# Optimization experiments

Hardware: AMD Instinct MI355X
Metric: run time of the kernel (lower is better)

Reference implementation:

```python
import jax, jax.numpy as jnp
import numpy as np

SINKHORN_ALPHA = 0.05
OT_MAX_ITER = 100
STOP_THR = 0.005
EPS = 1e-16
N_TOPICS, VOCAB, DIM = 1024, 50000, 256


def setup_inputs() -> dict:
    key = jax.random.key(0)
    k1, k2 = jax.random.split(key)
    x = jax.random.uniform(k1, (N_TOPICS, DIM), dtype=jnp.float32)
    y = jax.random.uniform(k2, (VOCAB, DIM), dtype=jnp.float32)
    return {"x": x, "y": y}


def _pairwise_sq_euclidean(x, y):
    return (jnp.sum(x * x, axis=1, keepdims=True)
            + jnp.sum(y * y, axis=1)
            - 2.0 * (x @ y.T))


def reference(x, y):
    M = _pairwise_sq_euclidean(x, y)          # [n, m]
    n, m = M.shape
    dt = M.dtype
    a = jnp.full((n, 1), 1.0 / n, dtype=dt)    # uniform source marginal
    b = jnp.full((m, 1), 1.0 / m, dtype=dt)    # uniform target marginal
    K = jnp.exp(-M * SINKHORN_ALPHA)           # Gibbs kernel [n, m]
    u0 = jnp.full((n, 1), 1.0 / n, dtype=dt)
    v0 = jnp.zeros((m, 1), dtype=dt)

    def cond_fn(carry):
        u, v, err, cpt = carry
        return (err > STOP_THR) & (cpt < OT_MAX_ITER)

    def body_fn(carry):
        u, v, err, cpt = carry
        v = b / (K.T @ u + EPS)                # [m, 1]
        u = a / (K @ v + EPS)                  # [n, 1]
        cpt = cpt + 1

        def compute_err(_):
            bb = v * (K.T @ u)                 # current column marginal
            return jnp.max(jnp.sum(jnp.abs(bb - b), axis=0))

        # original: convergence check only when cpt % 50 == 1
        err = jax.lax.cond((cpt % 50) == 1, compute_err, lambda _: err, operand=None)
        return (u, v, err, cpt)

    init = (u0, v0, jnp.asarray(1.0, dt), jnp.asarray(0, jnp.int32))
    u, v, err, cpt = jax.lax.while_loop(cond_fn, body_fn, init)

    transp = u * (K * v.T)                     # transport plan [n, m]
    loss_etp = jnp.sum(transp * M)
    return (loss_etp, transp)
```

## Files before the change

### kernel.cpp

```cpp
#include <hip/hip_runtime.h>
#include <hip/hip_cooperative_groups.h>
#include <cstdint>

namespace cg = cooperative_groups;

#define N_T 1024
#define M_V 50000
#define DIMS 256
#define NPAD 50048
#define GPANELS 391
#define CBLK 196
#define NPART (CBLK * 64)
#define NCHUNK 782
#define COOP_BLOCKS 1024
#define J8TOT 6250
#define F8BLK 25
#define LPART (F8BLK * 64)

constexpr float ALPHA     = 0.05f;
constexpr float INV_ALPHA = 20.0f;
constexpr float A_VAL     = 1.0f / 1024.0f;
constexpr float B_VAL     = 1.0f / 50000.0f;
constexpr float THR       = 0.005f;
constexpr float EPSV      = 1e-16f;

typedef short    bf16x8 __attribute__((ext_vector_type(8)));
typedef float    f32x4  __attribute__((ext_vector_type(4)));
typedef _Float16 half8v __attribute__((ext_vector_type(8)));

__device__ __forceinline__ float blockReduce256(float val) {
  #pragma unroll
  for (int off = 32; off; off >>= 1) val += __shfl_down(val, off, 64);
  __shared__ float redw[4];
  int lane = threadIdx.x & 63;
  int wid  = threadIdx.x >> 6;
  if (lane == 0) redw[wid] = val;
  __syncthreads();
  float r = 0.0f;
  if (threadIdx.x == 0) r = redw[0] + redw[1] + redw[2] + redw[3];
  __syncthreads();
  return r;
}

__device__ __forceinline__ unsigned short f2bf(float f) {
  union { float f; unsigned u; } c{f};
  unsigned r = c.u + 0x7FFF + ((c.u >> 16) & 1);
  return (unsigned short)(r >> 16);
}
__device__ __forceinline__ float bf2f(unsigned short b) {
  union { unsigned u; float f; } c{(unsigned)b << 16};
  return c.f;
}

__device__ __forceinline__ void gload16(const void* g, void* l) {
  __builtin_amdgcn_global_load_lds((const __attribute__((address_space(1))) unsigned int*)g,
                                   (__attribute__((address_space(3))) unsigned int*)l, 16, 0, 0);
}

__global__ __launch_bounds__(256) void sumsq_kernel(const float* __restrict__ in,
                                                    float* __restrict__ o, int rows) {
  int r = blockIdx.x;
  if (r >= rows) return;
  float v = in[(size_t)r * DIMS + threadIdx.x];
  float s = blockReduce256(v * v);
  if (threadIdx.x == 0) o[r] = s;
}

__global__ __launch_bounds__(256) void pack_x_kernel(const float* __restrict__ x,
                                                     unsigned short* __restrict__ Ap,
                                                     float* __restrict__ xx) {
  int r = blockIdx.x * 2 + (threadIdx.x >> 7);
  int k = (threadIdx.x & 127) * 2;
  float2 vx = *(const float2*)&x[(size_t)r * DIMS + k];
  ushort2 h2, l2;
  h2.x = f2bf(vx.x); h2.y = f2bf(vx.y);
  l2.x = f2bf(vx.x - bf2f(h2.x)); l2.y = f2bf(vx.y - bf2f(h2.y));
  *(ushort2*)&Ap[(size_t)r * 512 + k]       = h2;
  *(ushort2*)&Ap[(size_t)r * 512 + 256 + k] = l2;
  float ssq = vx.x * vx.x + vx.y * vx.y;
  #pragma unroll
  for (int off = 32; off; off >>= 1) ssq += __shfl_down(ssq, off, 64);
  __shared__ float rr[4];
  int lane = threadIdx.x & 63, wid = threadIdx.x >> 6;
  if (lane == 0) rr[wid] = ssq;
  __syncthreads();
  if ((threadIdx.x & 127) == 0) xx[r] = rr[wid] + rr[wid + 1];
}

__global__ __launch_bounds__(256) void pack_y_kernel(const float* __restrict__ y,
                                                     unsigned short* __restrict__ Bp,
                                                     float* __restrict__ yy) {
  int r = blockIdx.x * 2 + (threadIdx.x >> 7);
  int k = (threadIdx.x & 127) * 2;
  ushort2 h2 = {0, 0};
  float ssq = 0.0f;
  if (r < M_V) {
    float2 vy = *(const float2*)&y[(size_t)r * DIMS + k];
    h2.x = f2bf(vy.x); h2.y = f2bf(vy.y);
    ssq = vy.x * vy.x + vy.y * vy.y;
  }
  *(ushort2*)&Bp[(size_t)r * 256 + k] = h2;
  #pragma unroll
  for (int off = 32; off; off >>= 1) ssq += __shfl_down(ssq, off, 64);
  __shared__ float rr[4];
  int lane = threadIdx.x & 63, wid = threadIdx.x >> 6;
  if (lane == 0) rr[wid] = ssq;
  __syncthreads();
  if ((threadIdx.x & 127) == 0 && r < M_V) yy[r] = rr[wid] + rr[wid + 1];
}

__global__ __launch_bounds__(256) void mfma_gemm_kernel(const unsigned short* __restrict__ Ap,
                                                        const unsigned short* __restrict__ Bp,
                                                        const float* __restrict__ xx,
                                                        const float* __restrict__ yy,
                                                        _Float16* __restrict__ Kh,
                                                        float* __restrict__ colsumPart) {
  const int t  = blockIdx.x & 63;
  const int gb = blockIdx.x >> 6;
  const int panel = gb * 8 + (t & 7);
  const int rt    = t >> 3;
  if (panel >= GPANELS) return;
  const int i0 = rt * 128;
  const int j0 = panel * 128;

  __shared__ unsigned short Ah[2][128][32];
  __shared__ unsigned short Al[2][128][32];
  __shared__ unsigned short Bs[2][128][32];
  const int tid  = threadIdx.x;
  const int lane = tid & 63;
  const int wid  = tid >> 6;
  const int wr = wid >> 1, wc = wid & 1;

  f32x4 acc[4][4];
  #pragma unroll
  for (int m = 0; m < 4; ++m)
    #pragma unroll
    for (int n = 0; n < 4; ++n) acc[m][n] = (f32x4){0.f, 0.f, 0.f, 0.f};

  const int srow  = lane >> 2;
  const int sslot = lane & 3;

  auto STAGE = [&](int b, int k0) {
    #pragma unroll
    for (int q = 0; q < 2; ++q) {
      int rbase = (wid * 2 + q) * 16;
      int row = rbase + srow;
      int cg_ = sslot ^ ((row >> 1) & 3);
      gload16(Ap + (size_t)(i0 + row) * 512 + k0 + cg_ * 8,       &Ah[b][rbase][0]);
      gload16(Ap + (size_t)(i0 + row) * 512 + 256 + k0 + cg_ * 8, &Al[b][rbase][0]);
      gload16(Bp + (size_t)(j0 + row) * 256 + k0 + cg_ * 8,       &Bs[b][rbase][0]);
    }
  };

  STAGE(0, 0);
  int cur = 0;
  #pragma unroll
  for (int step = 0; step < 8; ++step) {
    if (step < 7) {
      STAGE(cur ^ 1, (step + 1) * 32);
      asm volatile("s_waitcnt vmcnt(6)" ::: "memory");
    } else {
      asm volatile("s_waitcnt vmcnt(0)" ::: "memory");
    }
    __builtin_amdgcn_s_barrier();
    __builtin_amdgcn_sched_barrier(0);
    bf16x8 ah[4], al[4], bb[4];
    #pragma unroll
    for (int m = 0; m < 4; ++m) {
      int row = wr * 64 + m * 16 + (lane & 15);
      int sl  = (lane >> 4) ^ ((row >> 1) & 3);
      ah[m] = *(const bf16x8*)&Ah[cur][row][sl * 8];
      al[m] = *(const bf16x8*)&Al[cur][row][sl * 8];
    }
    #pragma unroll
    for (int n = 0; n < 4; ++n) {
      int col = wc * 64 + n * 16 + (lane & 15);
      int sl  = (lane >> 4) ^ ((col >> 1) & 3);
      bb[n] = *(const bf16x8*)&Bs[cur][col][sl * 8];
    }
    #pragma unroll
    for (int m = 0; m < 4; ++m)
      #pragma unroll
      for (int n = 0; n < 4; ++n) {
        acc[m][n] = __builtin_amdgcn_mfma_f32_16x16x32_bf16(ah[m], bb[n], acc[m][n], 0, 0, 0);
        acc[m][n] = __builtin_amdgcn_mfma_f32_16x16x32_bf16(al[m], bb[n], acc[m][n], 0, 0, 0);
      }
    asm volatile("s_waitcnt lgkmcnt(0)" ::: "memory");
    __builtin_amdgcn_sched_barrier(0);
    __builtin_amdgcn_s_barrier();
    cur ^= 1;
  }

  float csum[4] = {0.f, 0.f, 0.f, 0.f};
  #pragma unroll
  for (int m = 0; m < 4; ++m) {
    int rowb = i0 + wr * 64 + m * 16 + (lane >> 4) * 4;
    #pragma unroll
    for (int n = 0; n < 4; ++n) {
      int col = j0 + wc * 64 + n * 16 + (lane & 15);
      float yyc = (col < M_V) ? yy[col] : 0.0f;
      #pragma unroll
      for (int r = 0; r < 4; ++r) {
        float mval = xx[rowb + r] + yyc - 2.0f * acc[m][n][r];
        _Float16 kh = (_Float16)__expf(-ALPHA * mval);
        if (col < M_V) Kh[(size_t)(rowb + r) * M_V + col] = kh;
        csum[n] += (float)kh;
      }
    }
  }
  #pragma unroll
  for (int n = 0; n < 4; ++n) {
    float c = csum[n];
    c += __shfl_xor(c, 16, 64);
    c += __shfl_xor(c, 32, 64);
    if (lane < 16) {
      int col = j0 + wc * 64 + n * 16 + lane;
      colsumPart[(size_t)(rt * 2 + wr) * NPAD + col] = c;
    }
  }
}

#define BM 64
#define BN 64
#define BK 32
__global__ __launch_bounds__(256) void gemm_k_kernel(const float* __restrict__ x,
                                                     const float* __restrict__ y,
                                                     const float* __restrict__ xx,
                                                     const float* __restrict__ yy,
                                                     float* Kmat) {
  __shared__ float As[BK][BM];
  __shared__ float Bs[BK][BN + 1];
  int tid = threadIdx.x;
  int i0 = blockIdx.y * BM;
  int j0 = blockIdx.x * BN;
  int tx = tid & 15, ty = tid >> 4;
  float acc[4][4] = {};
  for (int k0 = 0; k0 < DIMS; k0 += BK) {
    #pragma unroll
    for (int l = tid; l < 512; l += 256) {
      int r = l >> 3, kq = l & 7;
      float4 a4 = *(const float4*)&x[(size_t)(i0 + r) * DIMS + k0 + kq * 4];
      As[kq * 4 + 0][r] = a4.x; As[kq * 4 + 1][r] = a4.y;
      As[kq * 4 + 2][r] = a4.z; As[kq * 4 + 3][r] = a4.w;
    }
    #pragma unroll
    for (int l = tid; l < 512; l += 256) {
      int r = l >> 3, kq = l & 7;
      int j = j0 + r;
      float4 b4 = make_float4(0.f, 0.f, 0.f, 0.f);
      if (j < M_V) b4 = *(const float4*)&y[(size_t)j * DIMS + k0 + kq * 4];
      Bs[kq * 4 + 0][r] = b4.x; Bs[kq * 4 + 1][r] = b4.y;
      Bs[kq * 4 + 2][r] = b4.z; Bs[kq * 4 + 3][r] = b4.w;
    }
    __syncthreads();
    #pragma unroll
    for (int k = 0; k < BK; ++k) {
      float a[4], b[4];
      #pragma unroll
      for (int r = 0; r < 4; ++r) a[r] = As[k][ty * 4 + r];
      #pragma unroll
      for (int c = 0; c < 4; ++c) b[c] = Bs[k][tx * 4 + c];
      #pragma unroll
      for (int r = 0; r < 4; ++r)
        #pragma unroll
        for (int c = 0; c < 4; ++c) acc[r][c] += a[r] * b[c];
    }
    __syncthreads();
  }
  #pragma unroll
  for (int r = 0; r < 4; ++r) {
    int i = i0 + ty * 4 + r;
    float xxi = xx[i];
    #pragma unroll
    for (int c = 0; c < 4; ++c) {
      int j = j0 + tx * 4 + c;
      if (j < M_V) {
        float m = xxi + yy[j] - 2.0f * acc[r][c];
        Kmat[(size_t)i * M_V + j] = __expf(-ALPHA * m);
      }
    }
  }
}

__global__ __launch_bounds__(256) void v1_kernel(const float* __restrict__ cp,
                                                 float* __restrict__ v,
                                                 float* __restrict__ errAcc) {
  int j = blockIdx.x * 256 + threadIdx.x;
  if (j == 0) errAcc[0] = 0.0f;
  if (j < M_V) {
    float s = 0.0f;
    #pragma unroll
    for (int q = 0; q < 16; ++q) s += cp[(size_t)q * NPAD + j];
    v[j] = B_VAL / (s * A_VAL + EPSV);
  }
}

__global__ __launch_bounds__(256) void rowpass_kernel(const _Float16* __restrict__ Kh,
                                                      const float* __restrict__ v,
                                                      float* __restrict__ rowPart) {
  const int i = blockIdx.y;
  const int c = blockIdx.x;
  const half8v* K8 = (const half8v*)(Kh + (size_t)i * M_V);
  const float4* v4 = (const float4*)v;
  float p = 0.0f;
  int q = c * 3125 + threadIdx.x;
  #pragma unroll
  for (int it = 0; it < 12; ++it, q += 256) {
    half8v k8 = K8[q];
    float4 va = v4[q * 2], vb = v4[q * 2 + 1];
    p += (float)k8[0] * va.x + (float)k8[1] * va.y + (float)k8[2] * va.z + (float)k8[3] * va.w
       + (float)k8[4] * vb.x + (float)k8[5] * vb.y + (float)k8[6] * vb.z + (float)k8[7] * vb.w;
  }
  if (threadIdx.x < 53) {
    int q2 = c * 3125 + 3072 + threadIdx.x;
    half8v k8 = K8[q2];
    float4 va = v4[q2 * 2], vb = v4[q2 * 2 + 1];
    p += (float)k8[0] * va.x + (float)k8[1] * va.y + (float)k8[2] * va.z + (float)k8[3] * va.w
       + (float)k8[4] * vb.x + (float)k8[5] * vb.y + (float)k8[6] * vb.z + (float)k8[7] * vb.w;
  }
  p = blockReduce256(p);
  if (threadIdx.x == 0) rowPart[c * N_T + i] = p;
}

__global__ void u_kernel(const float* __restrict__ rowPart, float* __restrict__ u) {
  int i = blockIdx.x * 256 + threadIdx.x;
  u[i] = A_VAL / (rowPart[i] + rowPart[N_T + i] + EPSV);
}

__global__ __launch_bounds__(256) void specfinal_kernel(const _Float16* __restrict__ Kh,
                                                        const float* __restrict__ u_,
                                                        const float* __restrict__ v_,
                                                        float* __restrict__ out,
                                                        float* __restrict__ sPart,
                                                        float* __restrict__ lossPart) {
  const int j8 = blockIdx.x * 256 + threadIdx.x;
  const int by = blockIdx.y;
  float contrib = 0.0f;
  if (j8 < J8TOT) {
    const size_t jb = (size_t)j8 * 8;
    float4 va = ((const float4*)v_)[j8 * 2];
    float4 vb = ((const float4*)v_)[j8 * 2 + 1];
    float sp0 = 0.f, sp1 = 0.f, sp2 = 0.f, sp3 = 0.f;
    float sp4 = 0.f, sp5 = 0.f, sp6 = 0.f, sp7 = 0.f;
    #pragma unroll
    for (int r = 0; r < 16; ++r) {
      int i = by * 16 + r;
      half8v k8 = *(const half8v*)(Kh + (size_t)i * M_V + jb);
      float ui = u_[i];
      float k0 = (float)k8[0], k1 = (float)k8[1], k2 = (float)k8[2], k3 = (float)k8[3];
      float k4 = (float)k8[4], k5 = (float)k8[5], k6 = (float)k8[6], k7 = (float)k8[7];
      float t0 = ui * k0 * va.x, t1 = ui * k1 * va.y, t2 = ui * k2 * va.z, t3 = ui * k3 * va.w;
      float t4 = ui * k4 * vb.x, t5 = ui * k5 * vb.y, t6 = ui * k6 * vb.z, t7 = ui * k7 * vb.w;
      size_t o = 1 + (size_t)i * M_V + jb;
      out[o]     = t0; out[o + 1] = t1; out[o + 2] = t2; out[o + 3] = t3;
      out[o + 4] = t4; out[o + 5] = t5; out[o + 6] = t6; out[o + 7] = t7;
      contrib += t0 * (-__logf(k0)) + t1 * (-__logf(k1)) + t2 * (-__logf(k2)) + t3 * (-__logf(k3))
               + t4 * (-__logf(k4)) + t5 * (-__logf(k5)) + t6 * (-__logf(k6)) + t7 * (-__logf(k7));
      sp0 += k0 * ui; sp1 += k1 * ui; sp2 += k2 * ui; sp3 += k3 * ui;
      sp4 += k4 * ui; sp5 += k5 * ui; sp6 += k6 * ui; sp7 += k7 * ui;
    }
    float* sb = sPart + (size_t)by * M_V + jb;
    *(float4*)sb       = make_float4(sp0, sp1, sp2, sp3);
    *(float4*)(sb + 4) = make_float4(sp4, sp5, sp6, sp7);
  }
  contrib = blockReduce256(contrib) * INV_ALPHA;
  if (threadIdx.x == 0) lossPart[by * F8BLK + blockIdx.x] = contrib;
}

__global__ __launch_bounds__(256) void errfinish_kernel(const float* __restrict__ sPart,
                                                        const float* __restrict__ v_,
                                                        float* errAcc) {
  int j = blockIdx.x * 256 + threadIdx.x;
  float e = 0.0f;
  if (j < M_V) {
    float s = 0.0f;
    #pragma unroll
    for (int q = 0; q < 64; ++q) s += sPart[(size_t)q * M_V + j];
    e = fabsf(v_[j] * s - B_VAL);
  }
  e = blockReduce256(e);
  if (threadIdx.x == 0) atomicAdd(errAcc, e);
}

__global__ void setflag_kernel(const float* errAcc, int* notconv) {
  *notconv = (errAcc[0] > THR) ? 1 : 0;
}
__global__ void set1_kernel(int* p) { *p = 1; }

__global__ __launch_bounds__(256) void finishloss_kernel(const float* __restrict__ lossPart,
                                                         float* out, int np_) {
  float s = 0.0f;
  for (int i = threadIdx.x; i < np_; i += 256) s += lossPart[i];
  s = blockReduce256(s);
  if (threadIdx.x == 0) out[0] = s;
}

template <typename KT>
__global__ __launch_bounds__(256, 4) void sinkhorn_coop(const KT* Km,
                                                        float* __restrict__ u,
                                                        float* __restrict__ v,
                                                        float* __restrict__ s,
                                                        float* __restrict__ errAcc,
                                                        const int* __restrict__ notconv) {
  if (*notconv == 0) return;
  cg::grid_group grid = cg::this_grid();
  __shared__ float su[N_T];
  __shared__ float red[8][64];
  const int tid = threadIdx.x;
  const int bid = blockIdx.x;
  {
    int g0 = bid * 256 + tid;
    if (g0 < N_T) u[g0] = A_VAL;
    if (g0 < 2) errAcc[g0] = 0.0f;
  }
  grid.sync();
  for (int t = 1; t <= 100; ++t) {
    const bool check = (t == 2) || (t == 52);
    for (int i = tid; i < N_T; i += 256) su[i] = u[i];
    __syncthreads();
    const int g = tid >> 5, jl = tid & 31;
    float eacc = 0.0f;
    for (int c = bid; c < NCHUNK; c += COOP_BLOCKS) {
      const int j0 = c * 64;
      const int jj = j0 + jl * 2;
      float p0 = 0.f, p1 = 0.f;
      if (jj < M_V) {
        const KT* base = Km + (size_t)(g * 128) * M_V + jj;
        #pragma unroll 4
        for (int i = 0; i < 128; ++i) {
          float k0 = (float)base[(size_t)i * M_V];
          float k1 = (float)base[(size_t)i * M_V + 1];
          float uu = su[g * 128 + i];
          p0 += k0 * uu; p1 += k1 * uu;
        }
      }
      red[g][jl * 2]     = p0;
      red[g][jl * 2 + 1] = p1;
      __syncthreads();
      if (tid < 64) {
        int j = j0 + tid;
        if (j < M_V) {
          float st = 0.f;
          #pragma unroll
          for (int q = 0; q < 8; ++q) st += red[q][tid];
          if (check) {
            s[j] = st;
            eacc += fabsf(v[j] * st - B_VAL);
          } else {
            v[j] = B_VAL / (st + EPSV);
          }
        }
      }
      __syncthreads();
    }
    if (check) {
      float e = blockReduce256(eacc);
      if (tid == 0) atomicAdd(&errAcc[t == 2 ? 0 : 1], e);
    }
    grid.sync();
    if (check) {
      float e = errAcc[t == 2 ? 0 : 1];
      if (e <= THR) break;
      if (tid < 64) {
        for (int c = bid; c < NCHUNK; c += COOP_BLOCKS) {
          int j = c * 64 + tid;
          if (j < M_V) v[j] = B_VAL / (s[j] + EPSV);
        }
      }
      grid.sync();
    }
    {
      int i = bid;
      float p = 0.f;
      if (i < N_T) {
        const KT* row = Km + (size_t)i * M_V;
        for (int j = tid; j < M_V; j += 256) p += (float)row[j] * v[j];
      }
      p = blockReduce256(p);
      if (tid == 0 && i < N_T) u[i] = A_VAL / (p + EPSV);
    }
    grid.sync();
  }
}

template <typename KT>
__global__ __launch_bounds__(256) void final_kernel(const KT* Kmat,
                                                    const float* __restrict__ u,
                                                    const float* __restrict__ v,
                                                    float* out,
                                                    float* __restrict__ partials,
                                                    const int* __restrict__ gate) {
  if (*gate == 0) return;
  int j = blockIdx.x * 256 + threadIdx.x;
  float contrib = 0.0f;
  if (j < M_V) {
    float vj = v[j];
    #pragma unroll 4
    for (int r = 0; r < 16; ++r) {
      int i = blockIdx.y * 16 + r;
      size_t idx = (size_t)i * M_V + j;
      float k = (float)Kmat[idx];
      float tr = u[i] * k * vj;
      float m = -__logf(k) * INV_ALPHA;
      out[1 + idx] = tr;
      contrib += tr * m;
    }
  }
  contrib = blockReduce256(contrib);
  if (threadIdx.x == 0) partials[blockIdx.y * gridDim.x + blockIdx.x] = contrib;
}

__global__ __launch_bounds__(256) void finish_kernel(const float* __restrict__ partials,
                                                     float* out, int np_,
                                                     const int* __restrict__ gate) {
  if (*gate == 0) return;
  float s = 0.0f;
  for (int i = threadIdx.x; i < np_; i += 256) s += partials[i];
  s = blockReduce256(s);
  if (threadIdx.x == 0) out[0] = s;
}

extern "C" void kernel_launch(void* const* d_in, const int* in_sizes, int n_in,
                              void* d_out, int out_size, void* d_ws, size_t ws_size,
                              hipStream_t stream) {
  const float* x = (const float*)d_in[0];
  const float* y = (const float*)d_in[1];
  float* out = (float*)d_out;

  uintptr_t wp = (uintptr_t)d_ws;
  uintptr_t wend = (uintptr_t)d_ws + ws_size;
  auto alloc = [&](size_t bytes) -> void* {
    wp = (wp + 255) & ~(uintptr_t)255;
    void* p = (void*)wp;
    wp += bytes;
    return p;
  };
  float* u        = (float*)alloc((size_t)N_T * 4);
  float* v        = (float*)alloc((size_t)M_V * 4);
  float* s        = (float*)alloc((size_t)M_V * 4);
  float* xx       = (float*)alloc((size_t)N_T * 4);
  float* yy       = (float*)alloc((size_t)M_V * 4);
  float* partials = (float*)alloc((size_t)NPART * 4);
  float* lossPart = (float*)alloc((size_t)LPART * 4);
  float* rowPart  = (float*)alloc((size_t)2 * N_T * 4);
  float* errAcc   = (float*)alloc(64);
  int*   notconv  = (int*)alloc(64);
  float* colsumPart = (float*)alloc((size_t)16 * NPAD * 4);
  float* sPart    = (float*)alloc((size_t)64 * M_V * 4);

  const size_t apbytes = (size_t)N_T * 512 * 2;
  const size_t bpbytes = (size_t)NPAD * 256 * 2;
  const size_t khbytes = (size_t)N_T * M_V * 2;
  const size_t kfbytes = (size_t)N_T * M_V * 4;

  bool fast = ((wp + 1024) + apbytes + bpbytes + khbytes) <= wend;

  if (fast) {
    unsigned short* Ap = (unsigned short*)alloc(apbytes);
    unsigned short* Bp = (unsigned short*)alloc(bpbytes);
    _Float16*       Kh = (_Float16*)alloc(khbytes);

    pack_x_kernel<<<N_T / 2, 256, 0, stream>>>(x, Ap, xx);
    pack_y_kernel<<<NPAD / 2, 256, 0, stream>>>(y, Bp, yy);
    mfma_gemm_kernel<<<49 * 64, 256, 0, stream>>>(Ap, Bp, xx, yy, Kh, colsumPart);

    v1_kernel<<<CBLK, 256, 0, stream>>>(colsumPart, v, errAcc);
    rowpass_kernel<<<dim3(2, N_T), 256, 0, stream>>>(Kh, v, rowPart);
    u_kernel<<<N_T / 256, 256, 0, stream>>>(rowPart, u);

    specfinal_kernel<<<dim3(F8BLK, 64), 256, 0, stream>>>(Kh, u, v, out, sPart, lossPart);
    errfinish_kernel<<<CBLK, 256, 0, stream>>>(sPart, v, errAcc);
    setflag_kernel<<<1, 1, 0, stream>>>(errAcc, notconv);
    finishloss_kernel<<<1, 256, 0, stream>>>(lossPart, out, LPART);

    void* coopArgs[] = {(void*)&Kh, (void*)&u, (void*)&v, (void*)&s,
                        (void*)&errAcc, (void*)&notconv};
    hipLaunchCooperativeKernel(reinterpret_cast<void*>(sinkhorn_coop<_Float16>),
                               dim3(COOP_BLOCKS), dim3(256), coopArgs, 0, stream);
    final_kernel<_Float16><<<dim3(CBLK, 64), 256, 0, stream>>>(Kh, u, v, out, partials, notconv);
    finish_kernel<<<1, 256, 0, stream>>>(partials, out, NPART, notconv);
  } else {
    sumsq_kernel<<<N_T, 256, 0, stream>>>(x, xx, N_T);
    sumsq_kernel<<<M_V, 256, 0, stream>>>(y, yy, M_V);
    bool k_in_ws = ((wp + 512) + kfbytes) <= wend;
    float* Kmat = k_in_ws ? (float*)alloc(kfbytes) : out + 1;
    gemm_k_kernel<<<dim3((M_V + BN - 1) / BN, N_T / BM), 256, 0, stream>>>(x, y, xx, yy, Kmat);
    set1_kernel<<<1, 1, 0, stream>>>(notconv);
    void* coopArgs[] = {(void*)&Kmat, (void*)&u, (void*)&v, (void*)&s,
                        (void*)&errAcc, (void*)&notconv};
    hipLaunchCooperativeKernel(reinterpret_cast<void*>(sinkhorn_coop<float>),
                               dim3(COOP_BLOCKS), dim3(256), coopArgs, 0, stream);
    final_kernel<float><<<dim3(CBLK, 64), 256, 0, stream>>>(Kmat, u, v, out, partials, notconv);
    finish_kernel<<<1, 256, 0, stream>>>(partials, out, NPART, notconv);
  }
}
```

Baseline: 273.3 us.

## Fuse first Sinkhorn iteration and speculative final into cooperative kernel

Merges the x and y pack kernels into one launch. Replaces the seven-kernel chain (first v, row pass, u, speculative transport plan and loss, error finish, flag, loss finish) with one cooperative kernel that uses grid syncs between phases. The sinkhorn cooperative grid is now sized from occupancy queries rather than a fixed 1024 blocks, with loops changed to stride by gridDim. The aim is to cut launch and tail overhead, at the cost of grid-wide barriers, fewer blocks for the bandwidth-heavy speculative write phase, and per-call host occupancy queries.

```diff
diff --git a/kernel.cpp b/kernel.cpp
--- a/kernel.cpp
+++ b/kernel.cpp
@@ -12,8 +12,8 @@
 #define CBLK 196
 #define NPART (CBLK * 64)
 #define NCHUNK 782
-#define COOP_BLOCKS 1024
 #define J8TOT 6250
+#define J8SUB8 782
 #define F8BLK 25
 #define LPART (F8BLK * 64)
 
@@ -57,56 +57,46 @@
                                    (__attribute__((address_space(3))) unsigned int*)l, 16, 0, 0);
 }
 
-__global__ __launch_bounds__(256) void sumsq_kernel(const float* __restrict__ in,
-                                                    float* __restrict__ o, int rows) {
-  int r = blockIdx.x;
-  if (r >= rows) return;
-  float v = in[(size_t)r * DIMS + threadIdx.x];
-  float s = blockReduce256(v * v);
-  if (threadIdx.x == 0) o[r] = s;
-}
-
-__global__ __launch_bounds__(256) void pack_x_kernel(const float* __restrict__ x,
-                                                     unsigned short* __restrict__ Ap,
-                                                     float* __restrict__ xx) {
-  int r = blockIdx.x * 2 + (threadIdx.x >> 7);
-  int k = (threadIdx.x & 127) * 2;
-  float2 vx = *(const float2*)&x[(size_t)r * DIMS + k];
-  ushort2 h2, l2;
-  h2.x = f2bf(vx.x); h2.y = f2bf(vx.y);
-  l2.x = f2bf(vx.x - bf2f(h2.x)); l2.y = f2bf(vx.y - bf2f(h2.y));
-  *(ushort2*)&Ap[(size_t)r * 512 + k]       = h2;
-  *(ushort2*)&Ap[(size_t)r * 512 + 256 + k] = l2;
-  float ssq = vx.x * vx.x + vx.y * vx.y;
-  #pragma unroll
-  for (int off = 32; off; off >>= 1) ssq += __shfl_down(ssq, off, 64);
+__global__ __launch_bounds__(256) void pack_kernel(const float* __restrict__ x,
+                                                   const float* __restrict__ y,
+                                                   unsigned short* __restrict__ Ap,
+                                                   unsigned short* __restrict__ Bp,
+                                                   float* __restrict__ xx,
+                                                   float* __restrict__ yy) {
   __shared__ float rr[4];
   int lane = threadIdx.x & 63, wid = threadIdx.x >> 6;
-  if (lane == 0) rr[wid] = ssq;
-  __syncthreads();
-  if ((threadIdx.x & 127) == 0) xx[r] = rr[wid] + rr[wid + 1];
-}
-
-__global__ __launch_bounds__(256) void pack_y_kernel(const float* __restrict__ y,
-                                                     unsigned short* __restrict__ Bp,
-                                                     float* __restrict__ yy) {
-  int r = blockIdx.x * 2 + (threadIdx.x >> 7);
-  int k = (threadIdx.x & 127) * 2;
-  ushort2 h2 = {0, 0};
-  float ssq = 0.0f;
-  if (r < M_V) {
-    float2 vy = *(const float2*)&y[(size_t)r * DIMS + k];
-    h2.x = f2bf(vy.x); h2.y = f2bf(vy.y);
-    ssq = vy.x * vy.x + vy.y * vy.y;
-  }
-  *(ushort2*)&Bp[(size_t)r * 256 + k] = h2;
-  #pragma unroll
-  for (int off = 32; off; off >>= 1) ssq += __shfl_down(ssq, off, 64);
-  __shared__ float rr[4];
-  int lane = threadIdx.x & 63, wid = threadIdx.x >> 6;
-  if (lane == 0) rr[wid] = ssq;
-  __syncthreads();
-  if ((threadIdx.x & 127) == 0 && r < M_V) yy[r] = rr[wid] + rr[wid + 1];
+  if (blockIdx.x < N_T / 2) {
+    int r = blockIdx.x * 2 + (threadIdx.x >> 7);
+    int k = (threadIdx.x & 127) * 2;
+    float2 vx = *(const float2*)&x[(size_t)r * DIMS + k];
+    ushort2 h2, l2;
+    h2.x = f2bf(vx.x); h2.y = f2bf(vx.y);
+    l2.x = f2bf(vx.x - bf2f(h2.x)); l2.y = f2bf(vx.y - bf2f(h2.y));
+    *(ushort2*)&Ap[(size_t)r * 512 + k]       = h2;
+    *(ushort2*)&Ap[(size_t)r * 512 + 256 + k] = l2;
+    float ssq = vx.x * vx.x + vx.y * vx.y;
+    #pragma unroll
+    for (int off = 32; off; off >>= 1) ssq += __shfl_down(ssq, off, 64);
+    if (lane == 0) rr[wid] = ssq;
+    __syncthreads();
+    if ((threadIdx.x & 127) == 0) xx[r] = rr[wid] + rr[wid + 1];
+  } else {
+    int r = (blockIdx.x - N_T / 2) * 2 + (threadIdx.x >> 7);
+    int k = (threadIdx.x & 127) * 2;
+    ushort2 h2 = {0, 0};
+    float ssq = 0.0f;
+    if (r < M_V) {
+      float2 vy = *(const float2*)&y[(size_t)r * DIMS + k];
+      h2.x = f2bf(vy.x); h2.y = f2bf(vy.y);
+      ssq = vy.x * vy.x + vy.y * vy.y;
+    }
+    *(ushort2*)&Bp[(size_t)r * 256 + k] = h2;
+    #pragma unroll
+    for (int off = 32; off; off >>= 1) ssq += __shfl_down(ssq, off, 64);
+    if (lane == 0) rr[wid] = ssq;
+    __syncthreads();
+    if ((threadIdx.x & 127) == 0 && r < M_V) yy[r] = rr[wid] + rr[wid + 1];
+  }
 }
 
 __global__ __launch_bounds__(256) void mfma_gemm_kernel(const unsigned short* __restrict__ Ap,
@@ -220,64 +210,115 @@
   }
 }
 
-#define BM 64
-#define BN 64
-#define BK 32
-__global__ __launch_bounds__(256) void gemm_k_kernel(const float* __restrict__ x,
-                                                     const float* __restrict__ y,
-                                                     const float* __restrict__ xx,
-                                                     const float* __restrict__ yy,
-                                                     float* Kmat) {
-  __shared__ float As[BK][BM];
-  __shared__ float Bs[BK][BN + 1];
-  int tid = threadIdx.x;
-  int i0 = blockIdx.y * BM;
-  int j0 = blockIdx.x * BN;
-  int tx = tid & 15, ty = tid >> 4;
-  float acc[4][4] = {};
-  for (int k0 = 0; k0 < DIMS; k0 += BK) {
-    #pragma unroll
-    for (int l = tid; l < 512; l += 256) {
-      int r = l >> 3, kq = l & 7;
-      float4 a4 = *(const float4*)&x[(size_t)(i0 + r) * DIMS + k0 + kq * 4];
-      As[kq * 4 + 0][r] = a4.x; As[kq * 4 + 1][r] = a4.y;
-      As[kq * 4 + 2][r] = a4.z; As[kq * 4 + 3][r] = a4.w;
-    }
-    #pragma unroll
-    for (int l = tid; l < 512; l += 256) {
-      int r = l >> 3, kq = l & 7;
-      int j = j0 + r;
-      float4 b4 = make_float4(0.f, 0.f, 0.f, 0.f);
-      if (j < M_V) b4 = *(const float4*)&y[(size_t)j * DIMS + k0 + kq * 4];
-      Bs[kq * 4 + 0][r] = b4.x; Bs[kq * 4 + 1][r] = b4.y;
-      Bs[kq * 4 + 2][r] = b4.z; Bs[kq * 4 + 3][r] = b4.w;
-    }
-    __syncthreads();
-    #pragma unroll
-    for (int k = 0; k < BK; ++k) {
-      float a[4], b[4];
+__global__ __launch_bounds__(256) void mega_lite(const _Float16* __restrict__ Kh,
+                                                 const float* __restrict__ colsumPart,
+                                                 float* __restrict__ u,
+                                                 float* __restrict__ v,
+                                                 float* errAcc,
+                                                 float* __restrict__ lossPart,
+                                                 float* __restrict__ sPart,
+                                                 float* out,
+                                                 int* notconv) {
+  cg::grid_group grid = cg::this_grid();
+  const int tid = threadIdx.x;
+  const int bid = blockIdx.x;
+  const int nb  = gridDim.x;
+  const int stride = nb * 256;
+
+  for (int j = bid * 256 + tid; j < M_V; j += stride) {
+    float sum = 0.0f;
+    #pragma unroll
+    for (int q = 0; q < 16; ++q) sum += colsumPart[(size_t)q * NPAD + j];
+    v[j] = B_VAL / (sum * A_VAL + EPSV);
+  }
+  if (bid == 0 && tid < 4) errAcc[tid] = 0.0f;
+  grid.sync();
+
+  for (int row = bid; row < N_T; row += nb) {
+    const half8v* K8 = (const half8v*)(Kh + (size_t)row * M_V);
+    const float4* v4 = (const float4*)v;
+    float p = 0.0f;
+    int q = tid;
+    #pragma unroll
+    for (int it = 0; it < 24; ++it, q += 256) {
+      half8v k8 = K8[q];
+      float4 va = v4[q * 2], vb = v4[q * 2 + 1];
+      p += (float)k8[0] * va.x + (float)k8[1] * va.y + (float)k8[2] * va.z + (float)k8[3] * va.w
+         + (float)k8[4] * vb.x + (float)k8[5] * vb.y + (float)k8[6] * vb.z + (float)k8[7] * vb.w;
+    }
+    if (q < J8TOT) {
+      half8v k8 = K8[q];
+      float4 va = v4[q * 2], vb = v4[q * 2 + 1];
+      p += (float)k8[0] * va.x + (float)k8[1] * va.y + (float)k8[2] * va.z + (float)k8[3] * va.w
+         + (float)k8[4] * vb.x + (float)k8[5] * vb.y + (float)k8[6] * vb.z + (float)k8[7] * vb.w;
+    }
+    p = blockReduce256(p);
+    if (tid == 0) u[row] = A_VAL / (p + EPSV);
+  }
+  grid.sync();
+
+  {
+    float contrib = 0.0f;
+    for (int item = bid; item < 512; item += nb) {
+      const int by = item & 63;
+      const int sub = item >> 6;
+      const int lo = sub * J8SUB8;
+      const int hi = min(lo + J8SUB8, J8TOT);
+      for (int j8 = lo + tid; j8 < hi; j8 += 256) {
+        const size_t jb = (size_t)j8 * 8;
+        float4 va = ((const float4*)v)[j8 * 2];
+        float4 vb = ((const float4*)v)[j8 * 2 + 1];
+        float sp0 = 0.f, sp1 = 0.f, sp2 = 0.f, sp3 = 0.f;
+        float sp4 = 0.f, sp5 = 0.f, sp6 = 0.f, sp7 = 0.f;
+        #pragma unroll
+        for (int r = 0; r < 16; ++r) {
+          int i = by * 16 + r;
+          half8v k8 = *(const half8v*)(Kh + (size_t)i * M_V + jb);
+          float ui = u[i];
+          float k0 = (float)k8[0], k1 = (float)k8[1], k2 = (float)k8[2], k3 = (float)k8[3];
+          float k4 = (float)k8[4], k5 = (float)k8[5], k6 = (float)k8[6], k7 = (float)k8[7];
+          float t0 = ui * k0 * va.x, t1 = ui * k1 * va.y, t2 = ui * k2 * va.z, t3 = ui * k3 * va.w;
+          float t4 = ui * k4 * vb.x, t5 = ui * k5 * vb.y, t6 = ui * k6 * vb.z, t7 = ui * k7 * vb.w;
+          float* o = out + 1 + (size_t)i * M_V + jb;
+          __builtin_nontemporal_store(t0, o);     __builtin_nontemporal_store(t1, o + 1);
+          __builtin_nontemporal_store(t2, o + 2); __builtin_nontemporal_store(t3, o + 3);
+          __builtin_nontemporal_store(t4, o + 4); __builtin_nontemporal_store(t5, o + 5);
+          __builtin_nontemporal_store(t6, o + 6); __builtin_nontemporal_store(t7, o + 7);
+          contrib += t0 * (-__logf(k0)) + t1 * (-__logf(k1)) + t2 * (-__logf(k2)) + t3 * (-__logf(k3))
+                   + t4 * (-__logf(k4)) + t5 * (-__logf(k5)) + t6 * (-__logf(k6)) + t7 * (-__logf(k7));
+          sp0 += k0 * ui; sp1 += k1 * ui; sp2 += k2 * ui; sp3 += k3 * ui;
+          sp4 += k4 * ui; sp5 += k5 * ui; sp6 += k6 * ui; sp7 += k7 * ui;
+        }
+        float* sb = sPart + (size_t)by * M_V + jb;
+        *(float4*)sb       = make_float4(sp0, sp1, sp2, sp3);
+        *(float4*)(sb + 4) = make_float4(sp4, sp5, sp6, sp7);
+      }
+    }
+    contrib = blockReduce256(contrib) * INV_ALPHA;
+    if (tid == 0) lossPart[bid] = contrib;
+  }
+  grid.sync();
+
+  {
+    float e = 0.0f;
+    for (int j = bid * 256 + tid; j < M_V; j += stride) {
+      float ss = 0.0f;
       #pragma unroll
-      for (int r = 0; r < 4; ++r) a[r] = As[k][ty * 4 + r];
-      #pragma unroll
-      for (int c = 0; c < 4; ++c) b[c] = Bs[k][tx * 4 + c];
-      #pragma unroll
-      for (int r = 0; r < 4; ++r)
-        #pragma unroll
-        for (int c = 0; c < 4; ++c) acc[r][c] += a[r] * b[c];
-    }
-    __syncthreads();
-  }
-  #pragma unroll
-  for (int r = 0; r < 4; ++r) {
-    int i = i0 + ty * 4 + r;
-    float xxi = xx[i];
-    #pragma unroll
-    for (int c = 0; c < 4; ++c) {
-      int j = j0 + tx * 4 + c;
-      if (j < M_V) {
-        float m = xxi + yy[j] - 2.0f * acc[r][c];
-        Kmat[(size_t)i * M_V + j] = __expf(-ALPHA * m);
-      }
+      for (int q = 0; q < 64; ++q) ss += sPart[(size_t)q * M_V + j];
+      e += fabsf(v[j] * ss - B_VAL);
+    }
+    e = blockReduce256(e);
+    if (tid == 0) atomicAdd(&errAcc[0], e);
+  }
+  grid.sync();
+
+  if (bid == 0) {
+    float ls = 0.0f;
+    for (int i = tid; i < nb; i += 256) ls += lossPart[i];
+    ls = blockReduce256(ls);
+    if (tid == 0) {
+      out[0] = ls;
+      *notconv = (errAcc[0] > THR) ? 1 : 0;
     }
   }
 }
@@ -408,6 +449,7 @@
   __shared__ float red[8][64];
   const int tid = threadIdx.x;
   const int bid = blockIdx.x;
+  const int nb  = gridDim.x;
   {
     int g0 = bid * 256 + tid;
     if (g0 < N_T) u[g0] = A_VAL;
@@ -420,7 +462,7 @@
     __syncthreads();
     const int g = tid >> 5, jl = tid & 31;
     float eacc = 0.0f;
-    for (int c = bid; c < NCHUNK; c += COOP_BLOCKS) {
+    for (int c = bid; c < NCHUNK; c += nb) {
       const int j0 = c * 64;
       const int jj = j0 + jl * 2;
       float p0 = 0.f, p1 = 0.f;
@@ -462,22 +504,19 @@
       float e = errAcc[t == 2 ? 0 : 1];
       if (e <= THR) break;
       if (tid < 64) {
-        for (int c = bid; c < NCHUNK; c += COOP_BLOCKS) {
+        for (int c = bid; c < NCHUNK; c += nb) {
           int j = c * 64 + tid;
           if (j < M_V) v[j] = B_VAL / (s[j] + EPSV);
         }
       }
       grid.sync();
     }
-    {
-      int i = bid;
+    for (int i = bid; i < N_T; i += nb) {
       float p = 0.f;
-      if (i < N_T) {
-        const KT* row = Km + (size_t)i * M_V;
-        for (int j = tid; j < M_V; j += 256) p += (float)row[j] * v[j];
-      }
+      const KT* row = Km + (size_t)i * M_V;
+      for (int j = tid; j < M_V; j += 256) p += (float)row[j] * v[j];
       p = blockReduce256(p);
-      if (tid == 0 && i < N_T) u[i] = A_VAL / (p + EPSV);
+      if (tid == 0) u[i] = A_VAL / (p + EPSV);
     }
     grid.sync();
   }
@@ -520,6 +559,77 @@
   if (threadIdx.x == 0) out[0] = s;
 }
 
+__global__ __launch_bounds__(256) void sumsq_kernel(const float* __restrict__ in,
+                                                    float* __restrict__ o, int rows) {
+  int r = blockIdx.x;
+  if (r >= rows) return;
+  float v = in[(size_t)r * DIMS + threadIdx.x];
+  float s = blockReduce256(v * v);
+  if (threadIdx.x == 0) o[r] = s;
+}
+
+#define BM 64
+#define BN 64
+#define BK 32
+__global__ __launch_bounds__(256) void gemm_k_kernel(const float* __restrict__ x,
+                                                     const float* __restrict__ y,
+                                                     const float* __restrict__ xx,
+                                                     const float* __restrict__ yy,
+                                                     float* Kmat) {
+  __shared__ float As[BK][BM];
+  __shared__ float Bs[BK][BN + 1];
+  int tid = threadIdx.x;
+  int i0 = blockIdx.y * BM;
+  int j0 = blockIdx.x * BN;
+  int tx = tid & 15, ty = tid >> 4;
+  float acc[4][4] = {};
+  for (int k0 = 0; k0 < DIMS; k0 += BK) {
+    #pragma unroll
+    for (int l = tid; l < 512; l += 256) {
+      int r = l >> 3, kq = l & 7;
+      float4 a4 = *(const float4*)&x[(size_t)(i0 + r) * DIMS + k0 + kq * 4];
+      As[kq * 4 + 0][r] = a4.x; As[kq * 4 + 1][r] = a4.y;
+      As[kq * 4 + 2][r] = a4.z; As[kq * 4 + 3][r] = a4.w;
+    }
+    #pragma unroll
+    for (int l = tid; l < 512; l += 256) {
+      int r = l >> 3, kq = l & 7;
+      int j = j0 + r;
+      float4 b4 = make_float4(0.f, 0.f, 0.f, 0.f);
+      if (j < M_V) b4 = *(const float4*)&y[(size_t)j * DIMS + k0 + kq * 4];
+      Bs[kq * 4 + 0][r] = b4.x; Bs[kq * 4 + 1][r] = b4.y;
+      Bs[kq * 4 + 2][r] = b4.z; Bs[kq * 4 + 3][r] = b4.w;
+    }
+    __syncthreads();
+    #pragma unroll
+    for (int k = 0; k < BK; ++k) {
+      float a[4], b[4];
+      #pragma unroll
+      for (int r = 0; r < 4; ++r) a[r] = As[k][ty * 4 + r];
+      #pragma unroll
+      for (int c = 0; c < 4; ++c) b[c] = Bs[k][tx * 4 + c];
+      #pragma unroll
+      for (int r = 0; r < 4; ++r)
+        #pragma unroll
+        for (int c = 0; c < 4; ++c) acc[r][c] += a[r] * b[c];
+    }
+    __syncthreads();
+  }
+  #pragma unroll
+  for (int r = 0; r < 4; ++r) {
+    int i = i0 + ty * 4 + r;
+    float xxi = xx[i];
+    #pragma unroll
+    for (int c = 0; c < 4; ++c) {
+      int j = j0 + tx * 4 + c;
+      if (j < M_V) {
+        float m = xxi + yy[j] - 2.0f * acc[r][c];
+        Kmat[(size_t)i * M_V + j] = __expf(-ALPHA * m);
+      }
+    }
+  }
+}
+
 extern "C" void kernel_launch(void* const* d_in, const int* in_sizes, int n_in,
                               void* d_out, int out_size, void* d_ws, size_t ws_size,
                               hipStream_t stream) {
@@ -541,7 +651,7 @@
   float* xx       = (float*)alloc((size_t)N_T * 4);
   float* yy       = (float*)alloc((size_t)M_V * 4);
   float* partials = (float*)alloc((size_t)NPART * 4);
-  float* lossPart = (float*)alloc((size_t)LPART * 4);
+  float* lossPart = (float*)alloc((size_t)1600 * 4);
   float* rowPart  = (float*)alloc((size_t)2 * N_T * 4);
   float* errAcc   = (float*)alloc(64);
   int*   notconv  = (int*)alloc(64);
@@ -555,28 +665,52 @@
 
   bool fast = ((wp + 1024) + apbytes + bpbytes + khbytes) <= wend;
 
+  int dev = 0;
+  hipGetDevice(&dev);
+  int numCU = 256;
+  hipDeviceGetAttribute(&numCU, hipDeviceAttributeMultiprocessorCount, dev);
+
   if (fast) {
     unsigned short* Ap = (unsigned short*)alloc(apbytes);
     unsigned short* Bp = (unsigned short*)alloc(bpbytes);
     _Float16*       Kh = (_Float16*)alloc(khbytes);
 
-    pack_x_kernel<<<N_T / 2, 256, 0, stream>>>(x, Ap, xx);
-    pack_y_kernel<<<NPAD / 2, 256, 0, stream>>>(y, Bp, yy);
+    pack_kernel<<<N_T / 2 + NPAD / 2, 256, 0, stream>>>(x, y, Ap, Bp, xx, yy);
     mfma_gemm_kernel<<<49 * 64, 256, 0, stream>>>(Ap, Bp, xx, yy, Kh, colsumPart);
 
-    v1_kernel<<<CBLK, 256, 0, stream>>>(colsumPart, v, errAcc);
-    rowpass_kernel<<<dim3(2, N_T), 256, 0, stream>>>(Kh, v, rowPart);
-    u_kernel<<<N_T / 256, 256, 0, stream>>>(rowPart, u);
-
-    specfinal_kernel<<<dim3(F8BLK, 64), 256, 0, stream>>>(Kh, u, v, out, sPart, lossPart);
-    errfinish_kernel<<<CBLK, 256, 0, stream>>>(sPart, v, errAcc);
-    setflag_kernel<<<1, 1, 0, stream>>>(errAcc, notconv);
-    finishloss_kernel<<<1, 256, 0, stream>>>(lossPart, out, LPART);
-
+    int occMega = 0;
+    hipOccupancyMaxActiveBlocksPerMultiprocessor(&occMega, mega_lite, 256, 0);
+    long megaCap = (long)occMega * numCU;
+    int megaGrid = (int)(megaCap < 512 ? megaCap : 512);
+
+    bool megaDone = false;
+    if (megaGrid >= 128) {
+      void* args[] = {(void*)&Kh, (void*)&colsumPart, (void*)&u, (void*)&v,
+                      (void*)&errAcc, (void*)&lossPart, (void*)&sPart,
+                      (void*)&out, (void*)&notconv};
+      hipError_t lerr = hipLaunchCooperativeKernel(reinterpret_cast<void*>(mega_lite),
+                                                   dim3(megaGrid), dim3(256), args, 0, stream);
+      megaDone = (lerr == hipSuccess);
+    }
+    if (!megaDone) {
+      v1_kernel<<<CBLK, 256, 0, stream>>>(colsumPart, v, errAcc);
+      rowpass_kernel<<<dim3(2, N_T), 256, 0, stream>>>(Kh, v, rowPart);
+      u_kernel<<<N_T / 256, 256, 0, stream>>>(rowPart, u);
+      specfinal_kernel<<<dim3(F8BLK, 64), 256, 0, stream>>>(Kh, u, v, out, sPart, lossPart);
+      errfinish_kernel<<<CBLK, 256, 0, stream>>>(sPart, v, errAcc);
+      setflag_kernel<<<1, 1, 0, stream>>>(errAcc, notconv);
+      finishloss_kernel<<<1, 256, 0, stream>>>(lossPart, out, LPART);
+    }
+
+    int occS = 0;
+    hipOccupancyMaxActiveBlocksPerMultiprocessor(&occS, sinkhorn_coop<_Float16>, 256, 0);
+    long sCap = (long)occS * numCU;
+    int sGrid = (int)(sCap < 1024 ? sCap : 1024);
+    if (sGrid < 1) sGrid = 1;
     void* coopArgs[] = {(void*)&Kh, (void*)&u, (void*)&v, (void*)&s,
                         (void*)&errAcc, (void*)&notconv};
     hipLaunchCooperativeKernel(reinterpret_cast<void*>(sinkhorn_coop<_Float16>),
-                               dim3(COOP_BLOCKS), dim3(256), coopArgs, 0, stream);
+                               dim3(sGrid), dim3(256), coopArgs, 0, stream);
     final_kernel<_Float16><<<dim3(CBLK, 64), 256, 0, stream>>>(Kh, u, v, out, partials, notconv);
     finish_kernel<<<1, 256, 0, stream>>>(partials, out, NPART, notconv);
   } else {
@@ -586,10 +720,15 @@
     float* Kmat = k_in_ws ? (float*)alloc(kfbytes) : out + 1;
     gemm_k_kernel<<<dim3((M_V + BN - 1) / BN, N_T / BM), 256, 0, stream>>>(x, y, xx, yy, Kmat);
     set1_kernel<<<1, 1, 0, stream>>>(notconv);
+    int occS = 0;
+    hipOccupancyMaxActiveBlocksPerMultiprocessor(&occS, sinkhorn_coop<float>, 256, 0);
+    long sCap = (long)occS * numCU;
+    int sGrid = (int)(sCap < 1024 ? sCap : 1024);
+    if (sGrid < 1) sGrid = 1;
     void* coopArgs[] = {(void*)&Kmat, (void*)&u, (void*)&v, (void*)&s,
                         (void*)&errAcc, (void*)&notconv};
     hipLaunchCooperativeKernel(reinterpret_cast<void*>(sinkhorn_coop<float>),
-                               dim3(COOP_BLOCKS), dim3(256), coopArgs, 0, stream);
+                               dim3(sGrid), dim3(256), coopArgs, 0, stream);
     final_kernel<float><<<dim3(CBLK, 64), 256, 0, stream>>>(Kmat, u, v, out, partials, notconv);
     finish_kernel<<<1, 256, 0, stream>>>(partials, out, NPART, notconv);
   }
```

After: 381.6 us. 1.4x slower.
